# Performance work log

Measured on AMD Instinct MI355X. Metric: run time of the kernel, lower is better.

## Reference

```python
import jax, jax.numpy as jnp
import numpy as np

MAX_ITER = 3          # module init arg max_iter
FILL = 1e9            # large finite value for out-of-grid / out-of-label-range padding

N, H, W, C = 1, 320, 640, 32
NUM_DIR = 4


def setup_inputs() -> dict:
    key = jax.random.key(0)
    k1, k2, k3 = jax.random.split(key, 3)
    prob_vol = jax.random.uniform(k1, (N, H, W, C), dtype=jnp.float32)
    edge_weights = jax.random.uniform(k2, (N, NUM_DIR, H, W), dtype=jnp.float32)
    # affinities[:, :, :2] ~ L1 jump costs, affinities[:, :, 2] ~ L2 truncation cost
    affinities = jax.random.uniform(k3, (N, NUM_DIR, 3, H, W), dtype=jnp.float32)
    offset = jnp.zeros((N, NUM_DIR, H, W), dtype=jnp.float32)
    messages = jnp.zeros((N, NUM_DIR, H, W, C), dtype=jnp.float32)
    return {"prob_vol": prob_vol, "edge_weights": edge_weights,
            "affinities": affinities, "offset": offset, "messages": messages}


def _shift(x, axis, step):
    # result[p] = x[p - step] along `axis`, FILL outside the grid
    n = x.shape[axis]
    pw = [(0, 0)] * x.ndim
    if step > 0:
        pw[axis] = (step, 0)
        return jax.lax.slice_in_dim(jnp.pad(x, pw, constant_values=FILL), 0, n, axis=axis)
    pw[axis] = (0, -step)
    return jax.lax.slice_in_dim(jnp.pad(x, pw, constant_values=FILL), -step, n - step, axis=axis)


def _bp_iter(cost, edge, aff, offset, messages):
    # cost: (N,H,W,C); messages: (N,4,H,W,C); edge/offset: (N,4,H,W); aff: (N,4,3,H,W)
    total = cost + messages.sum(axis=1)  # belief pre-message, (N,H,W,C)
    # direction d: (d, opposite, spatial axis, step of sender->receiver)
    DIRS = [(0, 1, 2, 1), (1, 0, 2, -1), (2, 3, 1, 1), (3, 2, 1, -1)]
    new = []
    for d, opp, axis, step in DIRS:
        h = total - messages[:, opp]          # exclude reverse-direction message at sender
        hs = _shift(h, axis, step)            # sender's h aligned to receiver pixel
        w = edge[:, d][..., None]             # (N,H,W,1) edge weight
        if d % 2 == 0:
            a_m1 = aff[:, d, 0][..., None]    # cost for label jump -1
            a_p1 = aff[:, d, 1][..., None]    # cost for label jump +1
        else:  # opposite direction swaps the asymmetric +/-1 jump costs
            a_m1 = aff[:, d, 1][..., None]
            a_p1 = aff[:, d, 0][..., None]
        L2 = aff[:, d, 2][..., None]          # truncation cost for |jump| >= 2
        off = offset[:, d][..., None]
        big = jnp.full(hs.shape[:-1] + (1,), FILL, hs.dtype)
        h_lm1 = jnp.concatenate([big, hs[..., :-1]], axis=-1)  # hs(l-1)
        h_lp1 = jnp.concatenate([hs[..., 1:], big], axis=-1)   # hs(l+1)
        hmin = hs.min(axis=-1, keepdims=True)
        # min-sum update with truncated-linear pairwise: min over jump 0, +-1, truncated
        m = jnp.minimum(jnp.minimum(hs, h_lm1 + w * a_p1),
                        jnp.minimum(h_lp1 + w * a_m1, hmin + w * L2)) + w * off
        m = m - m.min(axis=-1, keepdims=True)  # message rescaling (message_scale)
        # boundary pixels have no sender -> zero message
        if d == 0:
            m = m.at[:, :, 0, :].set(0.0)
        elif d == 1:
            m = m.at[:, :, -1, :].set(0.0)
        elif d == 2:
            m = m.at[:, 0, :, :].set(0.0)
        else:
            m = m.at[:, -1, :, :].set(0.0)
        new.append(m)
    return jnp.stack(new, axis=1)


def reference(prob_vol, edge_weights, affinities, offset, messages):
    cost = -prob_vol
    for _ in range(MAX_ITER):
        messages = _bp_iter(cost, edge_weights, affinities, offset, messages)
    beliefs = messages.sum(axis=1) + cost
    beliefs = jax.nn.softmax(-beliefs, axis=-1)  # TemperatureSoftmin(dim=3, T=1)
    return beliefs, messages
```

## Files before the change

kernel.cpp:

```cpp
#include <hip/hip_runtime.h>
#include <math.h>

#define H 320
#define W 640
#define C 32
#define HW (H * W)
#define HWC (H * W * C)
#define FILLV 1e9f

#define TX 8
#define TY 8
#define EXT_X (TX + 2)
#define EXT_Y (TY + 2)
#define N_EXT (EXT_X * EXT_Y)
#define PSTR 36


__device__ __forceinline__ float group_min8(float v) {
    v = fminf(v, __shfl_xor(v, 4, 8));
    v = fminf(v, __shfl_xor(v, 2, 8));
    v = fminf(v, __shfl_xor(v, 1, 8));
    return v;
}
__device__ __forceinline__ float group_max8(float v) {
    v = fmaxf(v, __shfl_xor(v, 4, 8));
    v = fmaxf(v, __shfl_xor(v, 2, 8));
    v = fmaxf(v, __shfl_xor(v, 1, 8));
    return v;
}
__device__ __forceinline__ float group_sum8(float v) {
    v += __shfl_xor(v, 4, 8);
    v += __shfl_xor(v, 2, 8);
    v += __shfl_xor(v, 1, 8);
    return v;
}

__device__ __forceinline__ void msg_core_m1(
    float h0, float h1, float h2, float h3, int q,
    float wgt, float am1, float ap1, float l2c, float off,
    float& m0, float& m1, float& m2, float& m3)
{
    const float w_p1 = wgt * ap1;
    const float w_m1 = wgt * am1;
    const float w_L2 = wgt * l2c;
    const float w_of = wgt * off;

    const float up = __shfl_up(h3, 1, 8);
    const float dn = __shfl_down(h0, 1, 8);
    const float lm0 = (q == 0) ? FILLV : up;
    const float lp3 = (q == 7) ? FILLV : dn;

    float hmin = fminf(fminf(h0, h1), fminf(h2, h3));
    hmin = group_min8(hmin);
    const float tr = hmin + w_L2;

    m0 = fminf(fminf(h0, lm0 + w_p1), fminf(h1 + w_m1, tr)) + w_of;
    m1 = fminf(fminf(h1, h0  + w_p1), fminf(h2 + w_m1, tr)) + w_of;
    m2 = fminf(fminf(h2, h1  + w_p1), fminf(h3 + w_m1, tr)) + w_of;
    m3 = fminf(fminf(h3, h2  + w_p1), fminf(lp3 + w_m1, tr)) + w_of;
}

__device__ __forceinline__ void msg_core_r(
    float h0, float h1, float h2, float h3, int q,
    float wgt, float am1, float ap1, float l2c,
    float& m0, float& m1, float& m2, float& m3)
{
    const float w_p1 = wgt * ap1;
    const float w_m1 = wgt * am1;
    const float w_L2 = wgt * l2c;

    const float up = __shfl_up(h3, 1, 8);
    const float dn = __shfl_down(h0, 1, 8);
    const float lm0 = (q == 0) ? FILLV : up;
    const float lp3 = (q == 7) ? FILLV : dn;

    float hmin = fminf(fminf(h0, h1), fminf(h2, h3));
    hmin = group_min8(hmin);
    const float tr = hmin + w_L2;

    m0 = fminf(fminf(h0, lm0 + w_p1), fminf(h1 + w_m1, tr)) - hmin;
    m1 = fminf(fminf(h1, h0  + w_p1), fminf(h2 + w_m1, tr)) - hmin;
    m2 = fminf(fminf(h2, h1  + w_p1), fminf(h3 + w_m1, tr)) - hmin;
    m3 = fminf(fminf(h3, h2  + w_p1), fminf(lp3 + w_m1, tr)) - hmin;
}

__device__ __forceinline__ bool sender_of(int x, int y, int d, int& sx, int& sy) {
    sx = x; sy = y;
    if (d == 0) { sx = x - 1; return x == 0; }
    if (d == 1) { sx = x + 1; return x == W - 1; }
    if (d == 2) { sy = y - 1; return y == 0; }
    sy = y + 1; return y == H - 1;
}

__global__ __launch_bounds__(512) void bp_fused12_lds(
    const float* __restrict__ prob_vol,
    const float* __restrict__ edge,
    const float* __restrict__ aff,
    const float* __restrict__ offs,
    float* __restrict__ m2_out,
    float* __restrict__ T2_out)
{
    __shared__ float hbuf[4 * TX * TY * PSTR];

    const int bx0 = blockIdx.x * TX;
    const int by0 = blockIdx.y * TY;
    const int tid = threadIdx.x;
    const int q = tid & 7;
    const int lbase = 4 * q;

    for (int task = tid; task < N_EXT * 8; task += 512) {
        const int e  = task >> 3;
        const int ex = e % EXT_X;
        const int ey = e / EXT_X;
        const int gx = bx0 + ex - 1;
        const int gy = by0 + ey - 1;
        if (gx < 0 || gx >= W || gy < 0 || gy >= H) continue;

        const int sp = gy * W + gx;
        const float4 cs = *(const float4*)(prob_vol + sp * C + lbase);
        float t0 = -cs.x, t1 = -cs.y, t2 = -cs.z, t3 = -cs.w;
        float m1v[4][4];

        #pragma unroll
        for (int dd = 0; dd < 4; ++dd) {
            int s2x, s2y;
            const bool bnd = sender_of(gx, gy, dd, s2x, s2y);
            float u0 = 0.f, u1 = 0.f, u2 = 0.f, u3 = 0.f;
            if (!bnd) {
                const float4 c2 = *(const float4*)(prob_vol + (s2y * W + s2x) * C + lbase);
                const float wgt = edge[dd * HW + sp];
                const float A0  = aff[(dd * 3 + 0) * HW + sp];
                const float A1  = aff[(dd * 3 + 1) * HW + sp];
                const float L2c = aff[(dd * 3 + 2) * HW + sp];
                const float of  = offs[dd * HW + sp];
                const float am1 = ((dd & 1) == 0) ? A0 : A1;
                const float ap1 = ((dd & 1) == 0) ? A1 : A0;
                msg_core_m1(-c2.x, -c2.y, -c2.z, -c2.w, q,
                            wgt, am1, ap1, L2c, of, u0, u1, u2, u3);
            }
            m1v[dd][0] = u0; m1v[dd][1] = u1; m1v[dd][2] = u2; m1v[dd][3] = u3;
            t0 += u0; t1 += u1; t2 += u2; t3 += u3;
        }

        #pragma unroll
        for (int dd = 0; dd < 4; ++dd) {
            const int rx = gx + ((dd == 0) ? -1 : (dd == 1) ? 1 : 0);
            const int ry = gy + ((dd == 2) ? -1 : (dd == 3) ? 1 : 0);
            const int ix = rx - bx0, iy = ry - by0;
            if (ix >= 0 && ix < TX && iy >= 0 && iy < TY) {
                const int ip = iy * TX + ix;
                const int dp = dd ^ 1;
                float4 hv;
                hv.x = t0 - m1v[dd][0]; hv.y = t1 - m1v[dd][1];
                hv.z = t2 - m1v[dd][2]; hv.w = t3 - m1v[dd][3];
                *(float4*)&hbuf[(dp * TX * TY + ip) * PSTR + lbase] = hv;
            }
        }
    }

    __syncthreads();

    const int ip = tid >> 3;
    const int ix = ip & (TX - 1);
    const int iy = ip >> 3;
    const int gx = bx0 + ix;
    const int gy = by0 + iy;
    const int p  = gy * W + gx;

    float b0 = 0.f, b1 = 0.f, b2 = 0.f, b3 = 0.f;

    #pragma unroll
    for (int d = 0; d < 4; ++d) {
        const bool bnd = (d == 0 && gx == 0) || (d == 1 && gx == W - 1) ||
                         (d == 2 && gy == 0) || (d == 3 && gy == H - 1);
        float m0 = 0.f, m1 = 0.f, m2v = 0.f, m3v = 0.f;
        if (!bnd) {
            const float4 h4 = *(const float4*)&hbuf[(d * TX * TY + ip) * PSTR + lbase];
            const float wgt = edge[d * HW + p];
            const float A0  = aff[(d * 3 + 0) * HW + p];
            const float A1  = aff[(d * 3 + 1) * HW + p];
            const float L2c = aff[(d * 3 + 2) * HW + p];
            const float am1 = ((d & 1) == 0) ? A0 : A1;
            const float ap1 = ((d & 1) == 0) ? A1 : A0;
            msg_core_r(h4.x, h4.y, h4.z, h4.w, q, wgt, am1, ap1, L2c,
                       m0, m1, m2v, m3v);
        }
        float4 mv; mv.x = m0; mv.y = m1; mv.z = m2v; mv.w = m3v;
        *(float4*)(m2_out + d * HWC + p * C + lbase) = mv;
        b0 += m0; b1 += m1; b2 += m2v; b3 += m3v;
    }

    const float4 cown = *(const float4*)(prob_vol + p * C + lbase);
    float4 tv; tv.x = b0 - cown.x; tv.y = b1 - cown.y;
    tv.z = b2 - cown.z; tv.w = b3 - cown.w;
    *(float4*)(T2_out + p * C + lbase) = tv;
}

__global__ __launch_bounds__(256) void bp_iter3_kernel(
    const float* __restrict__ prob_vol,
    const float* __restrict__ edge,
    const float* __restrict__ aff,
    const float* __restrict__ T2,
    const float* __restrict__ m2,
    float* __restrict__ msg_out,
    float* __restrict__ beliefs)
{
    const int tid = blockIdx.x * blockDim.x + threadIdx.x;
    const int q = tid & 7;
    const int p = tid >> 3;
    if (p >= HW) return;
    const int y = p / W;
    const int x = p - y * W;
    const int lbase = 4 * q;

    float b0 = 0.f, b1 = 0.f, b2 = 0.f, b3 = 0.f;

    #pragma unroll
    for (int d = 0; d < 4; ++d) {
        const int opp = d ^ 1;
        int sx, sy;
        const bool bnd = sender_of(x, y, d, sx, sy);

        float m0 = 0.f, m1 = 0.f, m2v = 0.f, m3v = 0.f;
        if (!bnd) {
            const int sb = (sy * W + sx) * C + lbase;
            const float4 tv = *(const float4*)(T2 + sb);
            const float4 ov = *(const float4*)(m2 + opp * HWC + sb);
            const float h0 = tv.x - ov.x, h1 = tv.y - ov.y,
                        h2 = tv.z - ov.z, h3 = tv.w - ov.w;

            const float wgt = edge[d * HW + p];
            const float A0  = aff[(d * 3 + 0) * HW + p];
            const float A1  = aff[(d * 3 + 1) * HW + p];
            const float L2c = aff[(d * 3 + 2) * HW + p];
            const float am1 = ((d & 1) == 0) ? A0 : A1;
            const float ap1 = ((d & 1) == 0) ? A1 : A0;
            msg_core_r(h0, h1, h2, h3, q, wgt, am1, ap1, L2c,
                       m0, m1, m2v, m3v);
        }
        float4 mv; mv.x = m0; mv.y = m1; mv.z = m2v; mv.w = m3v;
        *(float4*)(msg_out + d * HWC + p * C + lbase) = mv;
        b0 += m0; b1 += m1; b2 += m2v; b3 += m3v;
    }

    const float4 cv = *(const float4*)(prob_vol + p * C + lbase);
    float t0 = cv.x - b0, t1 = cv.y - b1, t2 = cv.z - b2, t3 = cv.w - b3;
    float tmax = fmaxf(fmaxf(t0, t1), fmaxf(t2, t3));
    tmax = group_max8(tmax);
    const float e0 = __expf(t0 - tmax), e1 = __expf(t1 - tmax),
                e2 = __expf(t2 - tmax), e3 = __expf(t3 - tmax);
    float s = (e0 + e1) + (e2 + e3);
    s = group_sum8(s);
    const float inv = 1.0f / s;
    float4 bv; bv.x = e0 * inv; bv.y = e1 * inv; bv.z = e2 * inv; bv.w = e3 * inv;
    *(float4*)(beliefs + p * C + lbase) = bv;
}

extern "C" void kernel_launch(void* const* d_in, const int* in_sizes, int n_in,
                              void* d_out, int out_size, void* d_ws, size_t ws_size,
                              hipStream_t stream) {
    const float* prob_vol = (const float*)d_in[0];
    const float* edge     = (const float*)d_in[1];
    const float* aff      = (const float*)d_in[2];
    const float* offs     = (const float*)d_in[3];

    float* beliefs_out = (float*)d_out;
    float* msg_final   = (float*)d_out + HWC;
    float* m2          = (float*)d_ws;
    float* T2          = (float*)d_ws + 4 * HWC;

    const dim3 fblock(512);
    const dim3 fgrid(W / TX, H / TY);

    bp_fused12_lds<<<fgrid, fblock, 0, stream>>>(prob_vol, edge, aff, offs,
                                                 m2, T2);

    const dim3 block(256);
    const dim3 grid((HW * 8) / 256);
    bp_iter3_kernel<<<grid, block, 0, stream>>>(prob_vol, edge, aff,
                                                T2, m2, msg_final, beliefs_out);
}
```

Measured before the change: 305.7 us.

## Store per-direction sender beliefs between kernels and use DPP lane reductions

Result: faster. 291.6 us (-4.6%).

```diff
diff --git a/kernel.cpp b/kernel.cpp
--- a/kernel.cpp
+++ b/kernel.cpp
@@ -15,73 +15,56 @@
 #define N_EXT (EXT_X * EXT_Y)
 #define PSTR 36
 
-
-__device__ __forceinline__ float group_min8(float v) {
-    v = fminf(v, __shfl_xor(v, 4, 8));
-    v = fminf(v, __shfl_xor(v, 2, 8));
-    v = fminf(v, __shfl_xor(v, 1, 8));
+template <int CTRL>
+__device__ __forceinline__ float dppf(float x) {
+    int r = __builtin_amdgcn_update_dpp(0, __builtin_bit_cast(int, x),
+                                        CTRL, 0xF, 0xF, true);
+    return __builtin_bit_cast(float, r);
+}
+#define DPP_XOR1   0xB1
+#define DPP_XOR2   0x4E
+#define DPP_MIRR8  0x141
+#define DPP_UP1    0x111
+#define DPP_DN1    0x101
+
+__device__ __forceinline__ float gmin8(float v) {
+    v = fminf(v, dppf<DPP_XOR1>(v));
+    v = fminf(v, dppf<DPP_XOR2>(v));
+    v = fminf(v, dppf<DPP_MIRR8>(v));
     return v;
 }
-__device__ __forceinline__ float group_max8(float v) {
-    v = fmaxf(v, __shfl_xor(v, 4, 8));
-    v = fmaxf(v, __shfl_xor(v, 2, 8));
-    v = fmaxf(v, __shfl_xor(v, 1, 8));
+__device__ __forceinline__ float gmax8(float v) {
+    v = fmaxf(v, dppf<DPP_XOR1>(v));
+    v = fmaxf(v, dppf<DPP_XOR2>(v));
+    v = fmaxf(v, dppf<DPP_MIRR8>(v));
     return v;
 }
-__device__ __forceinline__ float group_sum8(float v) {
-    v += __shfl_xor(v, 4, 8);
-    v += __shfl_xor(v, 2, 8);
-    v += __shfl_xor(v, 1, 8);
+__device__ __forceinline__ float gsum8(float v) {
+    v += dppf<DPP_XOR1>(v);
+    v += dppf<DPP_XOR2>(v);
+    v += dppf<DPP_MIRR8>(v);
     return v;
 }
 
-__device__ __forceinline__ void msg_core_m1(
+template <bool RESCALE>
+__device__ __forceinline__ void msg_core(
     float h0, float h1, float h2, float h3, int q,
-    float wgt, float am1, float ap1, float l2c, float off,
+    float w_p1, float w_m1, float w_L2,
     float& m0, float& m1, float& m2, float& m3)
 {
-    const float w_p1 = wgt * ap1;
-    const float w_m1 = wgt * am1;
-    const float w_L2 = wgt * l2c;
-    const float w_of = wgt * off;
-
-    const float up = __shfl_up(h3, 1, 8);
-    const float dn = __shfl_down(h0, 1, 8);
+    const float up = dppf<DPP_UP1>(h3);
+    const float dn = dppf<DPP_DN1>(h0);
     const float lm0 = (q == 0) ? FILLV : up;
     const float lp3 = (q == 7) ? FILLV : dn;
 
-    float hmin = fminf(fminf(h0, h1), fminf(h2, h3));
-    hmin = group_min8(hmin);
+    float hmin = gmin8(fminf(fminf(h0, h1), fminf(h2, h3)));
     const float tr = hmin + w_L2;
-
-    m0 = fminf(fminf(h0, lm0 + w_p1), fminf(h1 + w_m1, tr)) + w_of;
-    m1 = fminf(fminf(h1, h0  + w_p1), fminf(h2 + w_m1, tr)) + w_of;
-    m2 = fminf(fminf(h2, h1  + w_p1), fminf(h3 + w_m1, tr)) + w_of;
-    m3 = fminf(fminf(h3, h2  + w_p1), fminf(lp3 + w_m1, tr)) + w_of;
-}
-
-__device__ __forceinline__ void msg_core_r(
-    float h0, float h1, float h2, float h3, int q,
-    float wgt, float am1, float ap1, float l2c,
-    float& m0, float& m1, float& m2, float& m3)
-{
-    const float w_p1 = wgt * ap1;
-    const float w_m1 = wgt * am1;
-    const float w_L2 = wgt * l2c;
-
-    const float up = __shfl_up(h3, 1, 8);
-    const float dn = __shfl_down(h0, 1, 8);
-    const float lm0 = (q == 0) ? FILLV : up;
-    const float lp3 = (q == 7) ? FILLV : dn;
-
-    float hmin = fminf(fminf(h0, h1), fminf(h2, h3));
-    hmin = group_min8(hmin);
-    const float tr = hmin + w_L2;
-
-    m0 = fminf(fminf(h0, lm0 + w_p1), fminf(h1 + w_m1, tr)) - hmin;
-    m1 = fminf(fminf(h1, h0  + w_p1), fminf(h2 + w_m1, tr)) - hmin;
-    m2 = fminf(fminf(h2, h1  + w_p1), fminf(h3 + w_m1, tr)) - hmin;
-    m3 = fminf(fminf(h3, h2  + w_p1), fminf(lp3 + w_m1, tr)) - hmin;
+    const float sub = RESCALE ? hmin : 0.f;
+
+    m0 = fminf(fminf(h0, lm0 + w_p1), fminf(h1 + w_m1, tr)) - sub;
+    m1 = fminf(fminf(h1, h0  + w_p1), fminf(h2 + w_m1, tr)) - sub;
+    m2 = fminf(fminf(h2, h1  + w_p1), fminf(h3 + w_m1, tr)) - sub;
+    m3 = fminf(fminf(h3, h2  + w_p1), fminf(lp3 + w_m1, tr)) - sub;
 }
 
 __device__ __forceinline__ bool sender_of(int x, int y, int d, int& sx, int& sy) {
@@ -96,9 +79,7 @@
     const float* __restrict__ prob_vol,
     const float* __restrict__ edge,
     const float* __restrict__ aff,
-    const float* __restrict__ offs,
-    float* __restrict__ m2_out,
-    float* __restrict__ T2_out)
+    float* __restrict__ h3op)
 {
     __shared__ float hbuf[4 * TX * TY * PSTR];
 
@@ -108,7 +89,10 @@
     const int q = tid & 7;
     const int lbase = 4 * q;
 
-    for (int task = tid; task < N_EXT * 8; task += 512) {
+    #pragma unroll
+    for (int r = 0; r < 2; ++r) {
+        const int task = tid + 512 * r;
+        if (task >= N_EXT * 8) break;
         const int e  = task >> 3;
         const int ex = e % EXT_X;
         const int ey = e / EXT_X;
@@ -132,11 +116,11 @@
                 const float A0  = aff[(dd * 3 + 0) * HW + sp];
                 const float A1  = aff[(dd * 3 + 1) * HW + sp];
                 const float L2c = aff[(dd * 3 + 2) * HW + sp];
-                const float of  = offs[dd * HW + sp];
                 const float am1 = ((dd & 1) == 0) ? A0 : A1;
                 const float ap1 = ((dd & 1) == 0) ? A1 : A0;
-                msg_core_m1(-c2.x, -c2.y, -c2.z, -c2.w, q,
-                            wgt, am1, ap1, L2c, of, u0, u1, u2, u3);
+                msg_core<false>(-c2.x, -c2.y, -c2.z, -c2.w, q,
+                                wgt * ap1, wgt * am1, wgt * L2c,
+                                u0, u1, u2, u3);
             }
             m1v[dd][0] = u0; m1v[dd][1] = u1; m1v[dd][2] = u2; m1v[dd][3] = u3;
             t0 += u0; t1 += u1; t2 += u2; t3 += u3;
@@ -167,13 +151,15 @@
     const int gy = by0 + iy;
     const int p  = gy * W + gx;
 
-    float b0 = 0.f, b1 = 0.f, b2 = 0.f, b3 = 0.f;
+    const float4 cown = *(const float4*)(prob_vol + p * C + lbase);
+    float t0 = -cown.x, t1 = -cown.y, t2 = -cown.z, t3 = -cown.w;
+    float m2v[4][4];
 
     #pragma unroll
     for (int d = 0; d < 4; ++d) {
         const bool bnd = (d == 0 && gx == 0) || (d == 1 && gx == W - 1) ||
                          (d == 2 && gy == 0) || (d == 3 && gy == H - 1);
-        float m0 = 0.f, m1 = 0.f, m2v = 0.f, m3v = 0.f;
+        float m0 = 0.f, m1 = 0.f, m2 = 0.f, m3 = 0.f;
         if (!bnd) {
             const float4 h4 = *(const float4*)&hbuf[(d * TX * TY + ip) * PSTR + lbase];
             const float wgt = edge[d * HW + p];
@@ -182,26 +168,27 @@
             const float L2c = aff[(d * 3 + 2) * HW + p];
             const float am1 = ((d & 1) == 0) ? A0 : A1;
             const float ap1 = ((d & 1) == 0) ? A1 : A0;
-            msg_core_r(h4.x, h4.y, h4.z, h4.w, q, wgt, am1, ap1, L2c,
-                       m0, m1, m2v, m3v);
-        }
-        float4 mv; mv.x = m0; mv.y = m1; mv.z = m2v; mv.w = m3v;
-        *(float4*)(m2_out + d * HWC + p * C + lbase) = mv;
-        b0 += m0; b1 += m1; b2 += m2v; b3 += m3v;
-    }
-
-    const float4 cown = *(const float4*)(prob_vol + p * C + lbase);
-    float4 tv; tv.x = b0 - cown.x; tv.y = b1 - cown.y;
-    tv.z = b2 - cown.z; tv.w = b3 - cown.w;
-    *(float4*)(T2_out + p * C + lbase) = tv;
+            msg_core<false>(h4.x, h4.y, h4.z, h4.w, q,
+                            wgt * ap1, wgt * am1, wgt * L2c, m0, m1, m2, m3);
+        }
+        m2v[d][0] = m0; m2v[d][1] = m1; m2v[d][2] = m2; m2v[d][3] = m3;
+        t0 += m0; t1 += m1; t2 += m2; t3 += m3;
+    }
+
+    #pragma unroll
+    for (int dd = 0; dd < 4; ++dd) {
+        float4 hv;
+        hv.x = t0 - m2v[dd][0]; hv.y = t1 - m2v[dd][1];
+        hv.z = t2 - m2v[dd][2]; hv.w = t3 - m2v[dd][3];
+        *(float4*)(h3op + (dd ^ 1) * HWC + p * C + lbase) = hv;
+    }
 }
 
 __global__ __launch_bounds__(256) void bp_iter3_kernel(
     const float* __restrict__ prob_vol,
     const float* __restrict__ edge,
     const float* __restrict__ aff,
-    const float* __restrict__ T2,
-    const float* __restrict__ m2,
+    const float* __restrict__ h3op,
     float* __restrict__ msg_out,
     float* __restrict__ beliefs)
 {
@@ -217,26 +204,21 @@
 
     #pragma unroll
     for (int d = 0; d < 4; ++d) {
-        const int opp = d ^ 1;
         int sx, sy;
         const bool bnd = sender_of(x, y, d, sx, sy);
 
         float m0 = 0.f, m1 = 0.f, m2v = 0.f, m3v = 0.f;
         if (!bnd) {
-            const int sb = (sy * W + sx) * C + lbase;
-            const float4 tv = *(const float4*)(T2 + sb);
-            const float4 ov = *(const float4*)(m2 + opp * HWC + sb);
-            const float h0 = tv.x - ov.x, h1 = tv.y - ov.y,
-                        h2 = tv.z - ov.z, h3 = tv.w - ov.w;
-
+            const float4 h4 = *(const float4*)(h3op + d * HWC + (sy * W + sx) * C + lbase);
             const float wgt = edge[d * HW + p];
             const float A0  = aff[(d * 3 + 0) * HW + p];
             const float A1  = aff[(d * 3 + 1) * HW + p];
             const float L2c = aff[(d * 3 + 2) * HW + p];
             const float am1 = ((d & 1) == 0) ? A0 : A1;
             const float ap1 = ((d & 1) == 0) ? A1 : A0;
-            msg_core_r(h0, h1, h2, h3, q, wgt, am1, ap1, L2c,
-                       m0, m1, m2v, m3v);
+            msg_core<true>(h4.x, h4.y, h4.z, h4.w, q,
+                           wgt * ap1, wgt * am1, wgt * L2c,
+                           m0, m1, m2v, m3v);
         }
         float4 mv; mv.x = m0; mv.y = m1; mv.z = m2v; mv.w = m3v;
         *(float4*)(msg_out + d * HWC + p * C + lbase) = mv;
@@ -245,12 +227,10 @@
 
     const float4 cv = *(const float4*)(prob_vol + p * C + lbase);
     float t0 = cv.x - b0, t1 = cv.y - b1, t2 = cv.z - b2, t3 = cv.w - b3;
-    float tmax = fmaxf(fmaxf(t0, t1), fmaxf(t2, t3));
-    tmax = group_max8(tmax);
+    float tmax = gmax8(fmaxf(fmaxf(t0, t1), fmaxf(t2, t3)));
     const float e0 = __expf(t0 - tmax), e1 = __expf(t1 - tmax),
                 e2 = __expf(t2 - tmax), e3 = __expf(t3 - tmax);
-    float s = (e0 + e1) + (e2 + e3);
-    s = group_sum8(s);
+    float s = gsum8((e0 + e1) + (e2 + e3));
     const float inv = 1.0f / s;
     float4 bv; bv.x = e0 * inv; bv.y = e1 * inv; bv.z = e2 * inv; bv.w = e3 * inv;
     *(float4*)(beliefs + p * C + lbase) = bv;
@@ -262,21 +242,18 @@
     const float* prob_vol = (const float*)d_in[0];
     const float* edge     = (const float*)d_in[1];
     const float* aff      = (const float*)d_in[2];
-    const float* offs     = (const float*)d_in[3];
 
     float* beliefs_out = (float*)d_out;
     float* msg_final   = (float*)d_out + HWC;
-    float* m2          = (float*)d_ws;
-    float* T2          = (float*)d_ws + 4 * HWC;
+    float* h3op        = (float*)d_ws;
 
     const dim3 fblock(512);
     const dim3 fgrid(W / TX, H / TY);
 
-    bp_fused12_lds<<<fgrid, fblock, 0, stream>>>(prob_vol, edge, aff, offs,
-                                                 m2, T2);
+    bp_fused12_lds<<<fgrid, fblock, 0, stream>>>(prob_vol, edge, aff, h3op);
 
     const dim3 block(256);
     const dim3 grid((HW * 8) / 256);
     bp_iter3_kernel<<<grid, block, 0, stream>>>(prob_vol, edge, aff,
-                                                T2, m2, msg_final, beliefs_out);
-}
+                                                h3op, msg_final, beliefs_out);
+}
```
